# Kernel tuning notes

Measured on AMD Instinct MI355X. Metric: run time of the kernel, lower is better.

## Reference

```python
import jax, jax.numpy as jnp
import numpy as np

NEG_SLOPE = 0.2  # PyG GATConv default negative_slope


def setup_inputs() -> dict:
    key = jax.random.key(0)
    ks = jax.random.split(key, 10)
    N, E, IN, H, C = 50000, 800000, 256, 4, 128
    return {
        "x": jax.random.normal(ks[0], (N, IN), jnp.float32),
        "edge_index": jax.random.randint(ks[1], (2, E), 0, N, jnp.int64),
        "W": jax.random.normal(ks[2], (IN, H * C), jnp.float32) * (1.0 / np.sqrt(IN)),
        "att_src": jax.random.normal(ks[3], (H, C), jnp.float32) * 0.1,
        "att_dst": jax.random.normal(ks[4], (H, C), jnp.float32) * 0.1,
        "gat_bias": jax.random.normal(ks[5], (C,), jnp.float32) * 0.01,
        "w1": jax.random.normal(ks[6], (C, C), jnp.float32) * (1.0 / np.sqrt(C)),
        "b1": jax.random.normal(ks[7], (C,), jnp.float32) * 0.01,
        "w2": jax.random.normal(ks[8], (C, 1), jnp.float32) * (1.0 / np.sqrt(C)),
        "b2": jax.random.normal(ks[9], (1,), jnp.float32) * 0.01,
    }


def _gat_conv(x, edge_index, W, att_src, att_dst, gat_bias):
    # PyG GATConv with concat=False (mean over heads), add_self_loops=True,
    # dropout inactive (eval mode).
    N = x.shape[0]
    H, C = att_src.shape
    xl = (x @ W).reshape(N, H, C)                       # [N,H,C] projected nodes
    a_src = jnp.einsum("nhc,hc->nh", xl, att_src)       # [N,H]
    a_dst = jnp.einsum("nhc,hc->nh", xl, att_dst)       # [N,H]
    loops = jnp.arange(N, dtype=edge_index.dtype)
    src = jnp.concatenate([edge_index[0], loops])        # [E+N]
    dst = jnp.concatenate([edge_index[1], loops])        # [E+N]
    logits = jax.nn.leaky_relu(a_src[src] + a_dst[dst], NEG_SLOPE)  # [E+N,H]
    # segment softmax over incoming edges of each dst node
    m = jax.ops.segment_max(logits, dst, num_segments=N)            # [N,H]
    e = jnp.exp(logits - m[dst])
    denom = jax.ops.segment_sum(e, dst, num_segments=N)             # [N,H]
    alpha = e / denom[dst]                                           # [E+N,H]
    # weighted scatter-add aggregation
    out = jax.ops.segment_sum(alpha[:, :, None] * xl[src], dst, num_segments=N)  # [N,H,C]
    return out.mean(axis=1) + gat_bias                   # concat=False -> head mean


def reference(x, edge_index, W, att_src, att_dst, gat_bias, w1, b1, w2, b2):
    h = _gat_conv(x, edge_index, W, att_src, att_dst, gat_bias)
    h = jax.nn.relu(h)
    h = jax.nn.relu(h @ w1 + b1)
    return (h @ w2 + b2)[:, 0]
```

## Files before the change

kernel.cpp:

```cpp
#include <hip/hip_runtime.h>
#include <hip/hip_bf16.h>


#define LEAKY(x) ((x) > 0.0f ? (x) : 0.2f * (x))
#define CAP 64

typedef __attribute__((ext_vector_type(8))) short short8v;
typedef __attribute__((ext_vector_type(4))) float floatx4;

__device__ __forceinline__ unsigned f2b(float f) {
    unsigned u = __float_as_uint(f);
    return (u + 0x7fffu + ((u >> 16) & 1u)) >> 16;
}

__device__ __forceinline__ void load_lds16(const void* g, void* lds) {
    __builtin_amdgcn_global_load_lds(
        (const __attribute__((address_space(1))) void*)g,
        (__attribute__((address_space(3))) void*)lds, 16, 0, 0);
}

__global__ __launch_bounds__(256) void prep_small(
    const float* __restrict__ W, const float* __restrict__ att_src,
    const float* __restrict__ att_dst, const float* __restrict__ w1,
    int* __restrict__ cnt, float* __restrict__ watt,
    ushort* __restrict__ WT2, ushort* __restrict__ w1t, int N) {
    int pb = blockIdx.x;
    int t = threadIdx.x;
    if (pb < 196) {
        int i = pb * 256 + t;
        if (i < N) cnt[i] = 0;
    } else if (pb < 204) {
        int idx = (pb - 196) * 256 + t;
        int k = idx >> 3;
        int h8 = idx & 7;
        int h = h8 & 3;
        const float* att = (h8 < 4) ? att_src : att_dst;
        const float* wrow = W + (size_t)k * 512 + h * 128;
        const float* arow = att + h * 128;
        float s = 0.f;
#pragma unroll 4
        for (int c = 0; c < 128; ++c) s += wrow[c] * arow[c];
        watt[h8 * 256 + k] = s;
    } else if (pb < 716) {
        int idx = (pb - 204) * 256 + t;
        int c = idx >> 10;
        int kk = idx & 1023;
        int h = kk >> 8, k = kk & 255;
        WT2[c * 1024 + kk] = (ushort)f2b(W[(size_t)k * 512 + h * 128 + c]);
    } else {
        int idx = (pb - 716) * 256 + t;
        int c = idx >> 7, k = idx & 127;
        w1t[c * 128 + k] = (ushort)f2b(w1[(size_t)k * 128 + c]);
    }
}

__global__ __launch_bounds__(256) void cast_score(
    const float* __restrict__ x, const float* __restrict__ watt,
    ushort* __restrict__ xb, float* __restrict__ asrc,
    float* __restrict__ adst, int N) {
    int w = threadIdx.x >> 6, l = threadIdx.x & 63;
    int n = blockIdx.x * 4 + w;
    if (n >= N) return;
    float4 xv = *(const float4*)(x + (size_t)n * 256 + l * 4);
    ushort4 ub;
    ub.x = (ushort)f2b(xv.x);
    ub.y = (ushort)f2b(xv.y);
    ub.z = (ushort)f2b(xv.z);
    ub.w = (ushort)f2b(xv.w);
    *(ushort4*)(xb + (size_t)n * 256 + l * 4) = ub;

    float acc[8];
#pragma unroll
    for (int h8 = 0; h8 < 8; ++h8) {
        float4 wv = *(const float4*)(watt + h8 * 256 + l * 4);
        acc[h8] = xv.x * wv.x + xv.y * wv.y + xv.z * wv.z + xv.w * wv.w;
    }
#pragma unroll
    for (int o = 32; o; o >>= 1)
#pragma unroll
        for (int h8 = 0; h8 < 8; ++h8) acc[h8] += __shfl_xor(acc[h8], o);
    if (l == 0) {
#pragma unroll
        for (int h = 0; h < 4; ++h) {
            asrc[n * 4 + h] = acc[h];
            adst[n * 4 + h] = acc[4 + h];
        }
    }
}

__global__ void fill_direct(const int* __restrict__ ei, int E, int N,
                            int* __restrict__ cnt, int* __restrict__ esrc,
                            const float* __restrict__ asrc,
                            const float* __restrict__ adst,
                            float4* __restrict__ wbuf) {
    int e = blockIdx.x * 256 + threadIdx.x;
    if (e >= E + N) return;
    int s, d;
    if (e < E) {
        s = ei[e];
        d = ei[E + e];
    } else {
        s = d = e - E;
    }
    if (d < 0 || d >= N || s < 0 || s >= N) return;
    int slot = atomicAdd(&cnt[d], 1);
    if (slot >= CAP) return;
    int pos = d * CAP + slot;
    esrc[pos] = s;
    float4 as = ((const float4*)asrc)[s];
    float4 ad = ((const float4*)adst)[d];
    float4 w;
    w.x = __expf(LEAKY(as.x + ad.x));
    w.y = __expf(LEAKY(as.y + ad.y));
    w.z = __expf(LEAKY(as.z + ad.z));
    w.w = __expf(LEAKY(as.w + ad.w));
    wbuf[pos] = w;
}

#define EDGE_FMA(wv, g)                                                      \
    {                                                                        \
        float _e0 = __uint_as_float((g).x << 16);                            \
        float _e1 = __uint_as_float((g).x & 0xffff0000u);                    \
        float _e2 = __uint_as_float((g).y << 16);                            \
        float _e3 = __uint_as_float((g).y & 0xffff0000u);                    \
        acc[0][0] += (wv).x * _e0; acc[0][1] += (wv).x * _e1;                \
        acc[0][2] += (wv).x * _e2; acc[0][3] += (wv).x * _e3;                \
        acc[1][0] += (wv).y * _e0; acc[1][1] += (wv).y * _e1;                \
        acc[1][2] += (wv).y * _e2; acc[1][3] += (wv).y * _e3;                \
        acc[2][0] += (wv).z * _e0; acc[2][1] += (wv).z * _e1;                \
        acc[2][2] += (wv).z * _e2; acc[2][3] += (wv).z * _e3;                \
        acc[3][0] += (wv).w * _e0; acc[3][1] += (wv).w * _e1;                \
        acc[3][2] += (wv).w * _e2; acc[3][3] += (wv).w * _e3;                \
        den0 += (wv).x; den1 += (wv).y; den2 += (wv).z; den3 += (wv).w;      \
    }

__global__ __launch_bounds__(256) void aggregate_x(
    const ushort* __restrict__ xb, const int* __restrict__ cnt,
    const int* __restrict__ esrc, const float4* __restrict__ wbuf,
    ushort* __restrict__ G, int N) {
    const int t = threadIdx.x;
    const int wv = t >> 6, l = t & 63;
    const int n = blockIdx.x * 4 + wv;
    if (n >= N) return;
    const int beg = n * CAP;
    const int deg = min(cnt[n], CAP);
    const uint loff = (uint)l * 4u;

    float acc[4][4];
#pragma unroll
    for (int h = 0; h < 4; ++h)
#pragma unroll
        for (int j = 0; j < 4; ++j) acc[h][j] = 0.f;
    float den0 = 0.f, den1 = 0.f, den2 = 0.f, den3 = 0.f;

    int i = 0;
    const int deg4 = deg & ~3;
    for (; i < deg4; i += 4) {
        int4 ss = *(const int4*)(esrc + beg + i);
        float4 w0 = wbuf[beg + i + 0], w1 = wbuf[beg + i + 1];
        float4 w2 = wbuf[beg + i + 2], w3 = wbuf[beg + i + 3];
        uint2 g0 = *(const uint2*)(xb + ((uint)ss.x * 256u + loff));
        uint2 g1 = *(const uint2*)(xb + ((uint)ss.y * 256u + loff));
        uint2 g2 = *(const uint2*)(xb + ((uint)ss.z * 256u + loff));
        uint2 g3 = *(const uint2*)(xb + ((uint)ss.w * 256u + loff));
        EDGE_FMA(w0, g0);
        EDGE_FMA(w1, g1);
        EDGE_FMA(w2, g2);
        EDGE_FMA(w3, g3);
    }
    for (; i < deg; ++i) {
        int s0 = esrc[beg + i];
        float4 w0 = wbuf[beg + i];
        uint2 g0 = *(const uint2*)(xb + ((uint)s0 * 256u + loff));
        EDGE_FMA(w0, g0);
    }

    float sc[4] = {0.25f / den0, 0.25f / den1, 0.25f / den2, 0.25f / den3};
#pragma unroll
    for (int h = 0; h < 4; ++h) {
        ushort4 o;
        o.x = (ushort)f2b(acc[h][0] * sc[h]);
        o.y = (ushort)f2b(acc[h][1] * sc[h]);
        o.z = (ushort)f2b(acc[h][2] * sc[h]);
        o.w = (ushort)f2b(acc[h][3] * sc[h]);
        *(ushort4*)(G + (size_t)n * 1024 + h * 256 + l * 4) = o;
    }
}

__global__ __launch_bounds__(256) void tail_kernel(
    const ushort* __restrict__ Gb,
    const ushort* __restrict__ Wstk,
    const ushort* __restrict__ w1t,
    const float* __restrict__ gat_bias, const float* __restrict__ b1,
    const float* __restrict__ w2, const float* __restrict__ b2,
    float* __restrict__ out, int N) {
    __shared__ char smem[65 * 1024];
    char* AlsB = smem;
    char* BlsB = smem + 16 * 1024;
    char* ndh = smem;
    char* w1ls = smem + 32 * 1024;
    float* sums = (float*)(smem + 64 * 1024);

    const int t = threadIdx.x;
    const int w = t >> 6;
    const int l = t & 63;
    const int wr = w >> 1, wc = w & 1;
    const int row0 = blockIdx.x * 128;

    float gbr[4], b1r[4], w2r[4];
#pragma unroll
    for (int n = 0; n < 4; ++n) {
        int cg = wc * 64 + n * 16 + (l & 15);
        gbr[n] = gat_bias[cg];
        b1r[n] = b1[cg];
        w2r[n] = w2[cg];
    }

    floatx4 acc[4][4];
#pragma unroll
    for (int m = 0; m < 4; ++m)
#pragma unroll
        for (int n = 0; n < 4; ++n) acc[m][n] = {0.f, 0.f, 0.f, 0.f};

    const int lr = l >> 3;
    const int kbyt = ((l & 7) ^ lr) << 4;
    const char* Abase = (const char*)Gb;
    const char* Bbase = (const char*)Wstk;

    for (int ks = 0; ks < 16; ++ks) {
        const int k0b = ks * 128;
#pragma unroll
        for (int c = 0; c < 4; ++c) {
            int rowt = w * 32 + c * 8 + lr;
            int rA = row0 + rowt;
            if (rA >= N) rA = N - 1;
            load_lds16(Abase + (size_t)rA * 2048 + k0b + kbyt,
                       AlsB + (w * 4 + c) * 1024);
            load_lds16(Bbase + (size_t)rowt * 2048 + k0b + kbyt,
                       BlsB + (w * 4 + c) * 1024);
        }
        __syncthreads();

#pragma unroll
        for (int kk = 0; kk < 2; ++kk) {
            const int kb_g = kk * 64 + (l >> 4) * 16;
            const int swz = (l & 7) << 4;
            short8v a[4], b[4];
#pragma unroll
            for (int m = 0; m < 4; ++m) {
                int row = wr * 64 + m * 16 + (l & 15);
                a[m] = *(const short8v*)(AlsB + row * 128 + (kb_g ^ swz));
            }
#pragma unroll
            for (int n = 0; n < 4; ++n) {
                int row = wc * 64 + n * 16 + (l & 15);
                b[n] = *(const short8v*)(BlsB + row * 128 + (kb_g ^ swz));
            }
#pragma unroll
            for (int m = 0; m < 4; ++m)
#pragma unroll
                for (int n = 0; n < 4; ++n)
                    acc[m][n] = __builtin_amdgcn_mfma_f32_16x16x32_bf16(
                        a[m], b[n], acc[m][n], 0, 0, 0);
        }
        __syncthreads();
    }

#pragma unroll
    for (int p = 0; p < 8; ++p) {
        int row = p * 16 + w * 4 + (l >> 4);
        int bcol = (l & 15) * 16;
        load_lds16((const char*)w1t + row * 256 + (bcol ^ ((row & 7) << 4)),
                   w1ls + p * 4096 + w * 1024);
    }
#pragma unroll
    for (int m = 0; m < 4; ++m) {
#pragma unroll
        for (int reg = 0; reg < 4; ++reg) {
            int r = wr * 64 + m * 16 + ((l >> 4) << 2) + reg;
            int srow = (r & 7) << 4;
#pragma unroll
            for (int n = 0; n < 4; ++n) {
                int c = wc * 64 + n * 16 + (l & 15);
                float v = acc[m][n][reg] + gbr[n];
                v = v > 0.f ? v : 0.f;
                *(ushort*)(ndh + r * 256 + ((2 * c) ^ srow)) = (ushort)f2b(v);
            }
        }
    }
    __syncthreads();

    floatx4 acc2[4][4];
#pragma unroll
    for (int m = 0; m < 4; ++m)
#pragma unroll
        for (int n = 0; n < 4; ++n) acc2[m][n] = {0.f, 0.f, 0.f, 0.f};

#pragma unroll
    for (int kk = 0; kk < 4; ++kk) {
        const int kb = kk * 64 + (l >> 4) * 16;
        short8v a2[4], b2f[4];
#pragma unroll
        for (int m = 0; m < 4; ++m) {
            int r = wr * 64 + m * 16 + (l & 15);
            a2[m] = *(const short8v*)(ndh + r * 256 + (kb ^ ((r & 7) << 4)));
        }
#pragma unroll
        for (int n = 0; n < 4; ++n) {
            int r = wc * 64 + n * 16 + (l & 15);
            b2f[n] = *(const short8v*)(w1ls + r * 256 + (kb ^ ((r & 7) << 4)));
        }
#pragma unroll
        for (int m = 0; m < 4; ++m)
#pragma unroll
            for (int n = 0; n < 4; ++n)
                acc2[m][n] = __builtin_amdgcn_mfma_f32_16x16x32_bf16(
                    a2[m], b2f[n], acc2[m][n], 0, 0, 0);
    }

    float part[4][4];
#pragma unroll
    for (int m = 0; m < 4; ++m)
#pragma unroll
        for (int reg = 0; reg < 4; ++reg) {
            float s = 0.f;
#pragma unroll
            for (int n = 0; n < 4; ++n) {
                float y = acc2[m][n][reg] + b1r[n];
                y = y > 0.f ? y : 0.f;
                s += y * w2r[n];
            }
            part[m][reg] = s;
        }
#pragma unroll
    for (int o = 1; o < 16; o <<= 1)
#pragma unroll
        for (int m = 0; m < 4; ++m)
#pragma unroll
            for (int reg = 0; reg < 4; ++reg)
                part[m][reg] += __shfl_xor(part[m][reg], o);
    if ((l & 15) == 0) {
#pragma unroll
        for (int m = 0; m < 4; ++m)
#pragma unroll
            for (int reg = 0; reg < 4; ++reg) {
                int r = wr * 64 + m * 16 + ((l >> 4) << 2) + reg;
                sums[wc * 128 + r] = part[m][reg];
            }
    }
    __syncthreads();
    if (t < 128) {
        int rg = row0 + t;
        if (rg < N) out[rg] = sums[t] + sums[128 + t] + b2[0];
    }
}

extern "C" void kernel_launch(void* const* d_in, const int* in_sizes, int n_in,
                              void* d_out, int out_size, void* d_ws,
                              size_t ws_size, hipStream_t stream) {
    const float* x = (const float*)d_in[0];
    const int* ei = (const int*)d_in[1];
    const float* W = (const float*)d_in[2];
    const float* att_src = (const float*)d_in[3];
    const float* att_dst = (const float*)d_in[4];
    const float* gat_bias = (const float*)d_in[5];
    const float* w1 = (const float*)d_in[6];
    const float* b1 = (const float*)d_in[7];
    const float* w2 = (const float*)d_in[8];
    const float* b2 = (const float*)d_in[9];
    float* out = (float*)d_out;

    const int N = in_sizes[0] / 256;
    const int E = in_sizes[1] / 2;

    size_t o = 0;
    char* wsb = (char*)d_ws;
    auto alloc = [&](size_t nbytes) -> void* {
        void* p = wsb + o;
        o += (nbytes + 255) & ~(size_t)255;
        return p;
    };
    float* asrc = (float*)alloc((size_t)N * 4 * 4);
    float* adst = (float*)alloc((size_t)N * 4 * 4);
    int* cnt = (int*)alloc((size_t)N * 4);
    int* esrc = (int*)alloc((size_t)N * CAP * 4);
    float4* wbuf = (float4*)alloc((size_t)N * CAP * 16);
    ushort* xb = (ushort*)alloc((size_t)N * 256 * 2);
    ushort* G = (ushort*)alloc((size_t)N * 1024 * 2);
    ushort* WT2 = (ushort*)alloc((size_t)128 * 1024 * 2);
    ushort* w1t = (ushort*)alloc((size_t)128 * 128 * 2);
    float* watt = (float*)alloc((size_t)8 * 256 * 4);

    prep_small<<<780, 256, 0, stream>>>(W, att_src, att_dst, w1, cnt, watt,
                                        WT2, w1t, N);
    cast_score<<<(N + 3) / 4, 256, 0, stream>>>(x, watt, xb, asrc, adst, N);
    fill_direct<<<(E + N + 255) / 256, 256, 0, stream>>>(ei, E, N, cnt, esrc,
                                                         asrc, adst, wbuf);
    aggregate_x<<<(N + 3) / 4, 256, 0, stream>>>(xb, cnt, esrc, wbuf, G, N);
    tail_kernel<<<(N + 127) / 128, 256, 0, stream>>>(
        G, WT2, w1t, gat_bias, b1, w2, b2, out, N);
}
```

Baseline: 192.3 us.

## Merge cast and edge fill into one launch; compute edge weights inside aggregation

The cast/score kernel and the edge bucketing kernel are merged into a single launch split by block index, since the fill no longer needs asrc/adst. Edge attention weights are no longer written to a per-slot float4 buffer. Instead, the aggregation wave loads one edge per lane, computes the exp weights, reduces the denominators with shuffles, and broadcasts source indices and weights via readlane. This removes a large intermediate write and read and one launch, in exchange for extra readlane and shuffle instructions in the aggregation loop.

```diff
diff --git a/kernel.cpp b/kernel.cpp
--- a/kernel.cpp
+++ b/kernel.cpp
@@ -11,6 +11,11 @@
 __device__ __forceinline__ unsigned f2b(float f) {
     unsigned u = __float_as_uint(f);
     return (u + 0x7fffu + ((u >> 16) & 1u)) >> 16;
+}
+
+__device__ __forceinline__ float rlf(float v, int i) {
+    return __uint_as_float(
+        __builtin_amdgcn_readlane(__float_as_uint(v), (unsigned)i));
 }
 
 __device__ __forceinline__ void load_lds16(const void* g, void* lds) {
@@ -54,90 +59,76 @@
     }
 }
 
-__global__ __launch_bounds__(256) void cast_score(
+__global__ __launch_bounds__(256) void cast_fill(
     const float* __restrict__ x, const float* __restrict__ watt,
     ushort* __restrict__ xb, float* __restrict__ asrc,
-    float* __restrict__ adst, int N) {
-    int w = threadIdx.x >> 6, l = threadIdx.x & 63;
-    int n = blockIdx.x * 4 + w;
-    if (n >= N) return;
-    float4 xv = *(const float4*)(x + (size_t)n * 256 + l * 4);
-    ushort4 ub;
-    ub.x = (ushort)f2b(xv.x);
-    ub.y = (ushort)f2b(xv.y);
-    ub.z = (ushort)f2b(xv.z);
-    ub.w = (ushort)f2b(xv.w);
-    *(ushort4*)(xb + (size_t)n * 256 + l * 4) = ub;
-
-    float acc[8];
-#pragma unroll
-    for (int h8 = 0; h8 < 8; ++h8) {
-        float4 wv = *(const float4*)(watt + h8 * 256 + l * 4);
-        acc[h8] = xv.x * wv.x + xv.y * wv.y + xv.z * wv.z + xv.w * wv.w;
-    }
-#pragma unroll
-    for (int o = 32; o; o >>= 1)
-#pragma unroll
-        for (int h8 = 0; h8 < 8; ++h8) acc[h8] += __shfl_xor(acc[h8], o);
-    if (l == 0) {
-#pragma unroll
-        for (int h = 0; h < 4; ++h) {
-            asrc[n * 4 + h] = acc[h];
-            adst[n * 4 + h] = acc[4 + h];
-        }
-    }
-}
-
-__global__ void fill_direct(const int* __restrict__ ei, int E, int N,
-                            int* __restrict__ cnt, int* __restrict__ esrc,
-                            const float* __restrict__ asrc,
-                            const float* __restrict__ adst,
-                            float4* __restrict__ wbuf) {
-    int e = blockIdx.x * 256 + threadIdx.x;
-    if (e >= E + N) return;
-    int s, d;
-    if (e < E) {
-        s = ei[e];
-        d = ei[E + e];
+    float* __restrict__ adst, const int* __restrict__ ei,
+    int* __restrict__ cnt, int* __restrict__ esrc, int N, int E, int CB) {
+    if ((int)blockIdx.x < CB) {
+        int w = threadIdx.x >> 6, l = threadIdx.x & 63;
+        int n = blockIdx.x * 4 + w;
+        if (n >= N) return;
+        float4 xv = *(const float4*)(x + (size_t)n * 256 + l * 4);
+        ushort4 ub;
+        ub.x = (ushort)f2b(xv.x);
+        ub.y = (ushort)f2b(xv.y);
+        ub.z = (ushort)f2b(xv.z);
+        ub.w = (ushort)f2b(xv.w);
+        *(ushort4*)(xb + (size_t)n * 256 + l * 4) = ub;
+
+        float acc[8];
+#pragma unroll
+        for (int h8 = 0; h8 < 8; ++h8) {
+            float4 wv = *(const float4*)(watt + h8 * 256 + l * 4);
+            acc[h8] = xv.x * wv.x + xv.y * wv.y + xv.z * wv.z + xv.w * wv.w;
+        }
+#pragma unroll
+        for (int o = 32; o; o >>= 1)
+#pragma unroll
+            for (int h8 = 0; h8 < 8; ++h8) acc[h8] += __shfl_xor(acc[h8], o);
+        if (l == 0) {
+#pragma unroll
+            for (int h = 0; h < 4; ++h) {
+                asrc[n * 4 + h] = acc[h];
+                adst[n * 4 + h] = acc[4 + h];
+            }
+        }
     } else {
-        s = d = e - E;
-    }
-    if (d < 0 || d >= N || s < 0 || s >= N) return;
-    int slot = atomicAdd(&cnt[d], 1);
-    if (slot >= CAP) return;
-    int pos = d * CAP + slot;
-    esrc[pos] = s;
-    float4 as = ((const float4*)asrc)[s];
-    float4 ad = ((const float4*)adst)[d];
-    float4 w;
-    w.x = __expf(LEAKY(as.x + ad.x));
-    w.y = __expf(LEAKY(as.y + ad.y));
-    w.z = __expf(LEAKY(as.z + ad.z));
-    w.w = __expf(LEAKY(as.w + ad.w));
-    wbuf[pos] = w;
-}
-
-#define EDGE_FMA(wv, g)                                                      \
+        int e = ((int)blockIdx.x - CB) * 256 + (int)threadIdx.x;
+        if (e >= E + N) return;
+        int s, d;
+        if (e < E) {
+            s = ei[e];
+            d = ei[E + e];
+        } else {
+            s = d = e - E;
+        }
+        if (d < 0 || d >= N || s < 0 || s >= N) return;
+        int slot = atomicAdd(&cnt[d], 1);
+        if (slot < CAP) esrc[d * CAP + slot] = s;
+    }
+}
+
+#define EDGE_FMA_S(wx, wy, wz, ww, g)                                        \
     {                                                                        \
         float _e0 = __uint_as_float((g).x << 16);                            \
         float _e1 = __uint_as_float((g).x & 0xffff0000u);                    \
         float _e2 = __uint_as_float((g).y << 16);                            \
         float _e3 = __uint_as_float((g).y & 0xffff0000u);                    \
-        acc[0][0] += (wv).x * _e0; acc[0][1] += (wv).x * _e1;                \
-        acc[0][2] += (wv).x * _e2; acc[0][3] += (wv).x * _e3;                \
-        acc[1][0] += (wv).y * _e0; acc[1][1] += (wv).y * _e1;                \
-        acc[1][2] += (wv).y * _e2; acc[1][3] += (wv).y * _e3;                \
-        acc[2][0] += (wv).z * _e0; acc[2][1] += (wv).z * _e1;                \
-        acc[2][2] += (wv).z * _e2; acc[2][3] += (wv).z * _e3;                \
-        acc[3][0] += (wv).w * _e0; acc[3][1] += (wv).w * _e1;                \
-        acc[3][2] += (wv).w * _e2; acc[3][3] += (wv).w * _e3;                \
-        den0 += (wv).x; den1 += (wv).y; den2 += (wv).z; den3 += (wv).w;      \
+        acc[0][0] += (wx) * _e0; acc[0][1] += (wx) * _e1;                    \
+        acc[0][2] += (wx) * _e2; acc[0][3] += (wx) * _e3;                    \
+        acc[1][0] += (wy) * _e0; acc[1][1] += (wy) * _e1;                    \
+        acc[1][2] += (wy) * _e2; acc[1][3] += (wy) * _e3;                    \
+        acc[2][0] += (wz) * _e0; acc[2][1] += (wz) * _e1;                    \
+        acc[2][2] += (wz) * _e2; acc[2][3] += (wz) * _e3;                    \
+        acc[3][0] += (ww) * _e0; acc[3][1] += (ww) * _e1;                    \
+        acc[3][2] += (ww) * _e2; acc[3][3] += (ww) * _e3;                    \
     }
 
 __global__ __launch_bounds__(256) void aggregate_x(
     const ushort* __restrict__ xb, const int* __restrict__ cnt,
-    const int* __restrict__ esrc, const float4* __restrict__ wbuf,
-    ushort* __restrict__ G, int N) {
+    const int* __restrict__ esrc, const float* __restrict__ asrc,
+    const float* __restrict__ adst, ushort* __restrict__ G, int N) {
     const int t = threadIdx.x;
     const int wv = t >> 6, l = t & 63;
     const int n = blockIdx.x * 4 + wv;
@@ -146,36 +137,67 @@
     const int deg = min(cnt[n], CAP);
     const uint loff = (uint)l * 4u;
 
+    float4 ad = ((const float4*)adst)[n];
+    int s_l = 0;
+    float4 wl = {0.f, 0.f, 0.f, 0.f};
+    if (l < deg) {
+        s_l = esrc[beg + l];
+        float4 as = ((const float4*)asrc)[s_l];
+        wl.x = __expf(LEAKY(as.x + ad.x));
+        wl.y = __expf(LEAKY(as.y + ad.y));
+        wl.z = __expf(LEAKY(as.z + ad.z));
+        wl.w = __expf(LEAKY(as.w + ad.w));
+    }
+    float dx = wl.x, dy = wl.y, dz = wl.z, dw = wl.w;
+#pragma unroll
+    for (int o = 32; o; o >>= 1) {
+        dx += __shfl_xor(dx, o);
+        dy += __shfl_xor(dy, o);
+        dz += __shfl_xor(dz, o);
+        dw += __shfl_xor(dw, o);
+    }
+    const float sc0 = 0.25f / dx, sc1 = 0.25f / dy;
+    const float sc2 = 0.25f / dz, sc3 = 0.25f / dw;
+
     float acc[4][4];
 #pragma unroll
     for (int h = 0; h < 4; ++h)
 #pragma unroll
         for (int j = 0; j < 4; ++j) acc[h][j] = 0.f;
-    float den0 = 0.f, den1 = 0.f, den2 = 0.f, den3 = 0.f;
 
     int i = 0;
     const int deg4 = deg & ~3;
     for (; i < deg4; i += 4) {
-        int4 ss = *(const int4*)(esrc + beg + i);
-        float4 w0 = wbuf[beg + i + 0], w1 = wbuf[beg + i + 1];
-        float4 w2 = wbuf[beg + i + 2], w3 = wbuf[beg + i + 3];
-        uint2 g0 = *(const uint2*)(xb + ((uint)ss.x * 256u + loff));
-        uint2 g1 = *(const uint2*)(xb + ((uint)ss.y * 256u + loff));
-        uint2 g2 = *(const uint2*)(xb + ((uint)ss.z * 256u + loff));
-        uint2 g3 = *(const uint2*)(xb + ((uint)ss.w * 256u + loff));
-        EDGE_FMA(w0, g0);
-        EDGE_FMA(w1, g1);
-        EDGE_FMA(w2, g2);
-        EDGE_FMA(w3, g3);
+        int s0 = __builtin_amdgcn_readlane(s_l, i + 0);
+        int s1 = __builtin_amdgcn_readlane(s_l, i + 1);
+        int s2 = __builtin_amdgcn_readlane(s_l, i + 2);
+        int s3 = __builtin_amdgcn_readlane(s_l, i + 3);
+        uint2 g0 = *(const uint2*)(xb + ((uint)s0 * 256u + loff));
+        uint2 g1 = *(const uint2*)(xb + ((uint)s1 * 256u + loff));
+        uint2 g2 = *(const uint2*)(xb + ((uint)s2 * 256u + loff));
+        uint2 g3 = *(const uint2*)(xb + ((uint)s3 * 256u + loff));
+        float w00 = rlf(wl.x, i + 0), w01 = rlf(wl.y, i + 0);
+        float w02 = rlf(wl.z, i + 0), w03 = rlf(wl.w, i + 0);
+        float w10 = rlf(wl.x, i + 1), w11 = rlf(wl.y, i + 1);
+        float w12 = rlf(wl.z, i + 1), w13 = rlf(wl.w, i + 1);
+        float w20 = rlf(wl.x, i + 2), w21 = rlf(wl.y, i + 2);
+        float w22 = rlf(wl.z, i + 2), w23 = rlf(wl.w, i + 2);
+        float w30 = rlf(wl.x, i + 3), w31 = rlf(wl.y, i + 3);
+        float w32 = rlf(wl.z, i + 3), w33 = rlf(wl.w, i + 3);
+        EDGE_FMA_S(w00, w01, w02, w03, g0);
+        EDGE_FMA_S(w10, w11, w12, w13, g1);
+        EDGE_FMA_S(w20, w21, w22, w23, g2);
+        EDGE_FMA_S(w30, w31, w32, w33, g3);
     }
     for (; i < deg; ++i) {
-        int s0 = esrc[beg + i];
-        float4 w0 = wbuf[beg + i];
+        int s0 = __builtin_amdgcn_readlane(s_l, i);
         uint2 g0 = *(const uint2*)(xb + ((uint)s0 * 256u + loff));
-        EDGE_FMA(w0, g0);
-    }
-
-    float sc[4] = {0.25f / den0, 0.25f / den1, 0.25f / den2, 0.25f / den3};
+        float w00 = rlf(wl.x, i), w01 = rlf(wl.y, i);
+        float w02 = rlf(wl.z, i), w03 = rlf(wl.w, i);
+        EDGE_FMA_S(w00, w01, w02, w03, g0);
+    }
+
+    const float sc[4] = {sc0, sc1, sc2, sc3};
 #pragma unroll
     for (int h = 0; h < 4; ++h) {
         ushort4 o;
@@ -384,19 +406,21 @@
     float* adst = (float*)alloc((size_t)N * 4 * 4);
     int* cnt = (int*)alloc((size_t)N * 4);
     int* esrc = (int*)alloc((size_t)N * CAP * 4);
-    float4* wbuf = (float4*)alloc((size_t)N * CAP * 16);
     ushort* xb = (ushort*)alloc((size_t)N * 256 * 2);
     ushort* G = (ushort*)alloc((size_t)N * 1024 * 2);
     ushort* WT2 = (ushort*)alloc((size_t)128 * 1024 * 2);
     ushort* w1t = (ushort*)alloc((size_t)128 * 128 * 2);
     float* watt = (float*)alloc((size_t)8 * 256 * 4);
 
+    const int CB = (N + 3) / 4;
+    const int FB = (E + N + 255) / 256;
+
     prep_small<<<780, 256, 0, stream>>>(W, att_src, att_dst, w1, cnt, watt,
                                         WT2, w1t, N);
-    cast_score<<<(N + 3) / 4, 256, 0, stream>>>(x, watt, xb, asrc, adst, N);
-    fill_direct<<<(E + N + 255) / 256, 256, 0, stream>>>(ei, E, N, cnt, esrc,
-                                                         asrc, adst, wbuf);
-    aggregate_x<<<(N + 3) / 4, 256, 0, stream>>>(xb, cnt, esrc, wbuf, G, N);
+    cast_fill<<<CB + FB, 256, 0, stream>>>(x, watt, xb, asrc, adst, ei, cnt,
+                                           esrc, N, E, CB);
+    aggregate_x<<<(N + 3) / 4, 256, 0, stream>>>(xb, cnt, esrc, asrc, adst, G,
+                                                 N);
     tail_kernel<<<(N + 127) / 128, 256, 0, stream>>>(
         G, WT2, w1t, gat_bias, b1, w2, b2, out, N);
 }
```

Measured after the change: 210.7 us. 9.5% more time.
